# Performance work log

Hardware: AMD Instinct MI355X
Metric: run time of the kernel (lower is better)

## Reference

```python
import jax, jax.numpy as jnp
import numpy as np
from jax import lax

# ---- config (mirrors cfg) ----
NUM_LEVELS = 4
DS = 2            # DS_FACTOR
T = 16            # TILE_SIZE
SR = 4            # SEARCH_RADIUS
PADD = 1
SW = 0.1          # SPATIAL_WEIGHT
GR = 2            # GAUSS_RADIUS
SIGMA = 1.0
SS = 2 * (SR + PADD) + 1      # 11: padded search grid
SSC = 2 * SR + 1              # 9: cropped search grid
WIN = T + 2 * (SR + PADD)     # 26: gathered window per tile

# ---- subpixel-refinement quadratic-fit filters (from __init__) ----
F_A11 = jnp.asarray(np.array([[1,-2,1],[2,-4,2],[1,-2,1]], np.float32) / 4.0)
F_A22 = jnp.asarray(np.array([[1,2,1],[-2,-4,-2],[1,2,1]], np.float32) / 4.0)
F_A12 = jnp.asarray(np.array([[1,0,-1],[0,0,0],[-1,0,1]], np.float32) / 4.0)
F_B1  = jnp.asarray(np.array([[-1,0,1],[-2,0,2],[-1,0,1]], np.float32) / 8.0)
F_B2  = jnp.asarray(np.array([[-1,-2,-1],[0,0,0],[1,2,1]], np.float32) / 8.0)
F_C   = jnp.asarray(np.array([[-1,2,-1],[2,12,2],[-1,2,-1]], np.float32) / 16.0)


def _gauss_kernel():
    ws = 2 * GR + 1
    ax = np.arange(ws, dtype=np.float32) - GR
    g = np.exp(-(ax ** 2) / (2.0 * SIGMA ** 2))
    k = np.outer(g, g)
    k = k / k.sum()
    return jnp.asarray(k, jnp.float32)


def _pyramid(x):
    """Gaussian pyramid: depthwise gaussian blur + avg-pool(ds) per level."""
    k = _gauss_kernel()[None, None]  # OIHW, C=1
    pad = (2 * GR + 1 - 1) // 2
    pyr = [x]
    for _ in range(NUM_LEVELS - 1):
        y = lax.conv_general_dilated(x, k, (1, 1), [(pad, pad), (pad, pad)],
                                     dimension_numbers=('NCHW', 'OIHW', 'NCHW'))
        n, c, h, w = y.shape
        x = y.reshape(n, c, h // DS, DS, w // DS, DS).mean(axis=(3, 5))
        pyr.append(x)
    return pyr


def _sdist_map():
    ax = (np.arange(SS, dtype=np.float32) - (SR + PADD)) / float(SS)
    return jnp.asarray(ax[:, None] ** 2 + ax[None, :] ** 2, jnp.float32)


def _step(init_offset, src, dst):
    """One pyramid-level block-matching step + subpixel refine."""
    n, nth, ntw, _ = init_offset.shape
    H, W = src.shape[2], src.shape[3]
    oy = jnp.round(init_offset[..., 0]).astype(jnp.int32)
    ox = jnp.round(init_offset[..., 1]).astype(jnp.int32)
    base_y = (jnp.arange(nth, dtype=jnp.int32) * T)[None, :, None]
    base_x = (jnp.arange(ntw, dtype=jnp.int32) * T)[None, None, :]
    y0 = base_y + oy - (SR + PADD)
    x0 = base_x + ox - (SR + PADD)
    Y = jnp.clip(y0[..., None] + jnp.arange(WIN), 0, H - 1)
    X = jnp.clip(x0[..., None] + jnp.arange(WIN), 0, W - 1)
    nidx = jnp.arange(n)[:, None, None, None, None]
    window = dst[:, 0][nidx, Y[..., :, None], X[..., None, :]]
    # source tiles [n,nth,ntw,T,T]
    src_t = src[:, 0].reshape(n, nth, T, ntw, T).transpose(0, 1, 3, 2, 4)
    # all SSxSS candidate tiles from the window (static slide indices)
    sl = jnp.arange(SS)[:, None] + jnp.arange(T)[None, :]  # [SS,T]
    cand = window[:, :, :, sl[:, None, :, None], sl[None, :, None, :]]  # [n,nth,ntw,SS,SS,T,T]
    adist = jnp.mean((cand - src_t[:, :, :, None, None]) ** 2, axis=(-2, -1))
    dist_full = adist + SW * _sdist_map()  # [n,nth,ntw,SS,SS]
    dist = dist_full[:, :, :, PADD:-PADD, PADD:-PADD].reshape(n, nth, ntw, SSC * SSC)
    min_dist = jnp.min(dist, axis=3)
    pk = jnp.argmin(dist, axis=3)
    py = pk // SSC
    px = pk % SSC
    offset = init_offset + jnp.stack([(py - SR).astype(jnp.float32),
                                      (px - SR).astype(jnp.float32)], axis=3)
    # RegionSelection: 3x3 neighborhood of dist_full around (py+PADD, px+PADD)
    ry = (py + PADD)[..., None] + jnp.arange(-1, 2)
    rx = (px + PADD)[..., None] + jnp.arange(-1, 2)
    tyi = jnp.arange(nth)[None, :, None, None, None]
    txi = jnp.arange(ntw)[None, None, :, None, None]
    yreg = dist_full[nidx, tyi, txi, ry[..., :, None], rx[..., None, :]]  # [n,nth,ntw,3,3]
    s = lambda f: jnp.sum(f * yreg, axis=(-2, -1))
    a11 = jax.nn.relu(s(F_A11))
    a22 = jax.nn.relu(s(F_A22))
    a12 = s(F_A12)
    b1 = s(F_B1)
    b2 = s(F_B2)
    det = a11 * a22 - a12 ** 2
    a12z = jnp.where(det < 0, jnp.zeros_like(a12), a12)
    mu_x = -(a22 * b1 - a12z * b2) / det
    mu_y = -(a11 * b2 - a12z * b1) / det
    mu_len = jnp.sqrt(mu_y ** 2 + mu_x ** 2)
    dx = jnp.where(mu_len < 1.0, mu_x, jnp.zeros_like(mu_x))
    dy = jnp.where(mu_len < 1.0, mu_y, jnp.zeros_like(mu_y))
    offset = offset.at[..., 0].add(dy).at[..., 1].add(dx)
    return offset, min_dist


def _inherit(prev_offset, nth, ntw, H, W):
    typ = jnp.arange(nth) // DS
    txp = jnp.arange(ntw) // DS
    off = DS * prev_offset[:, typ[:, None], txp[None, :], :]
    iy = (jnp.arange(nth, dtype=jnp.float32) * T)[None, :, None]
    ix = (jnp.arange(ntw, dtype=jnp.float32) * T)[None, None, :]
    dy = jnp.clip(off[..., 0] + iy, 0.0, float(H - T)) - iy
    dx = jnp.clip(off[..., 1] + ix, 0.0, float(W - T)) - ix
    return jnp.round(jnp.stack([dy, dx], axis=3))


def _align(src, dst):
    ps = _pyramid(src)
    pd = _pyramid(dst)
    offset = None
    min_dist = None
    for level in range(NUM_LEVELS - 1, -1, -1):
        s, d = ps[level], pd[level]
        n, _, h, w = s.shape
        nth = int(np.ceil(h / T))
        ntw = int(np.ceil(w / T))
        if level == NUM_LEVELS - 1:
            init = jnp.zeros((n, nth, ntw, 2), jnp.float32)
        else:
            init = _inherit(offset, nth, ntw, h, w)
        offset, min_dist = _step(init, s, d)
    # nearest-neighbor upsample by TILE_SIZE to per-pixel maps
    pixel_off = jnp.repeat(jnp.repeat(offset, T, axis=1), T, axis=2)   # [n,H,W,2]
    pixel_dist = jnp.repeat(jnp.repeat(min_dist, T, axis=1), T, axis=2)  # [n,H,W]
    return pixel_off, pixel_dist


def setup_inputs() -> dict:
    key = jax.random.key(0)
    k1, k2 = jax.random.split(key)
    src = jax.random.uniform(k1, (4, 1, 512, 512), jnp.float32)
    dst = jax.random.uniform(k2, (4, 1, 512, 512), jnp.float32)
    return {"src": src, "dst": dst}


def reference(src, dst):
    return _align(src, dst)
```

## Files before the change

### kernel.cpp

```cpp
#include <hip/hip_runtime.h>


#define NB 4
#define NPIX (NB * 512 * 512)

constexpr float H6[6] = {
    0.027244342f, 0.149345013f, 0.323410645f,
    0.323410645f, 0.149345013f, 0.027244342f
};

__global__ void __launch_bounds__(256, 4)
pyramid_kernel(const float* __restrict__ src, const float* __restrict__ dst,
               float* __restrict__ ws) {
    __shared__ float smem[5520];
    float* patch = smem;
    float* tmpH1 = smem + 3840;
    float* l1    = smem;
    float* tmpH2 = smem + 784;
    float* l2    = smem + 1120;
    float* tmpH3 = smem + 1264;

    float* sL1 = ws;
    float* dL1 = sL1 + 4 * 65536;
    float* sL2 = dL1 + 4 * 65536;
    float* dL2 = sL2 + 4 * 16384;
    float* sL3 = dL2 + 4 * 16384;
    float* dL3 = sL3 + 4 * 4096;

    const int bx = blockIdx.x, by = blockIdx.y, z = blockIdx.z;
    const int t = threadIdx.x;
    const float* in = (z < 4) ? (src + (size_t)z * 262144) : (dst + (size_t)(z - 4) * 262144);
    float* oL1 = ((z < 4) ? sL1 : dL1) + (size_t)(z & 3) * 65536;
    float* oL2 = ((z < 4) ? sL2 : dL2) + (size_t)(z & 3) * 16384;
    float* oL3 = ((z < 4) ? sL3 : dL3) + (size_t)(z & 3) * 4096;

    {
        const int oy = by * 32 - 14, ox = bx * 32 - 14;
        for (int idx = t; idx < 3600; idx += 256) {
            int r = idx / 60, c = idx - r * 60;
            int gy = oy + r, gx = ox + c;
            float v = 0.f;
            if ((unsigned)gy < 512u && (unsigned)gx < 512u) v = in[gy * 512 + gx];
            patch[r * 64 + c] = v;
        }
    }
    __syncthreads();
    for (int idx = t; idx < 1680; idx += 256) {
        int r = idx / 28, v = idx - r * 28;
        const float* p = &patch[r * 64 + 2 * v];
        float a = 0.f;
        #pragma unroll
        for (int bq = 0; bq < 6; ++bq) a = fmaf(H6[bq], p[bq], a);
        tmpH1[r * 28 + v] = a;
    }
    __syncthreads();
    {
        const int oy = by * 16 - 6, ox = bx * 16 - 6;
        for (int idx = t; idx < 784; idx += 256) {
            int u = idx / 28, v = idx - u * 28;
            float a = 0.f;
            int y1 = oy + u, x1 = ox + v;
            if ((unsigned)y1 < 256u && (unsigned)x1 < 256u) {
                #pragma unroll
                for (int bq = 0; bq < 6; ++bq) a = fmaf(H6[bq], tmpH1[(2 * u + bq) * 28 + v], a);
            }
            l1[u * 28 + v] = a;
        }
    }
    __syncthreads();
    {
        int u = t >> 4, v = t & 15;
        oL1[(by * 16 + u) * 256 + bx * 16 + v] = l1[(6 + u) * 28 + 6 + v];
    }
    for (int idx = t; idx < 336; idx += 256) {
        int r = idx / 12, v = idx - r * 12;
        const float* p = &l1[r * 28 + 2 * v];
        float a = 0.f;
        #pragma unroll
        for (int bq = 0; bq < 6; ++bq) a = fmaf(H6[bq], p[bq], a);
        tmpH2[r * 12 + v] = a;
    }
    __syncthreads();
    {
        const int oy = by * 8 - 2, ox = bx * 8 - 2;
        if (t < 144) {
            int u = t / 12, v = t - u * 12;
            float a = 0.f;
            int y2 = oy + u, x2 = ox + v;
            if ((unsigned)y2 < 128u && (unsigned)x2 < 128u) {
                #pragma unroll
                for (int bq = 0; bq < 6; ++bq) a = fmaf(H6[bq], tmpH2[(2 * u + bq) * 12 + v], a);
            }
            l2[u * 12 + v] = a;
        }
    }
    __syncthreads();
    if (t < 64) {
        int u = t >> 3, v = t & 7;
        oL2[(by * 8 + u) * 128 + bx * 8 + v] = l2[(2 + u) * 12 + 2 + v];
    } else if (t < 112) {
        int idx = t - 64;
        int r = idx >> 2, v = idx & 3;
        const float* p = &l2[r * 12 + 2 * v];
        float a = 0.f;
        #pragma unroll
        for (int bq = 0; bq < 6; ++bq) a = fmaf(H6[bq], p[bq], a);
        tmpH3[r * 4 + v] = a;
    }
    __syncthreads();
    if (t < 16) {
        int u = t >> 2, v = t & 3;
        float a = 0.f;
        #pragma unroll
        for (int bq = 0; bq < 6; ++bq) a = fmaf(H6[bq], tmpH3[(2 * u + bq) * 4 + v], a);
        oL3[(by * 4 + u) * 64 + bx * 4 + v] = a;
    }
}

template<bool FULL>
__device__ __forceinline__ void do_level(const float* __restrict__ simg,
                                         const float* __restrict__ dimg, int H,
                                         int ty, int tx, float pary, float parx, bool first,
                                         float* win, float* st, float* dist, int lt,
                                         float& roy, float& rox, float& rod) {
    constexpr int NL = FULL ? 256 : 128;

    float dyf = 0.f, dxf = 0.f;
    if (!first) {
        float iy = (float)(ty * 16), ix = (float)(tx * 16);
        dyf = rintf(fminf(fmaxf(2.f * pary + iy, 0.f), (float)(H - 16)) - iy);
        dxf = rintf(fminf(fmaxf(2.f * parx + ix, 0.f), (float)(H - 16)) - ix);
    }
    const int ioy = (int)dyf, iox = (int)dxf;
    const int y0 = ty * 16 + ioy - 5;
    const int x0 = tx * 16 + iox - 5;

    for (int idx = lt; idx < 676; idx += NL) {
        int r = idx / 26, c = idx - r * 26;
        int gy = min(max(y0 + r, 0), H - 1);
        int gx = min(max(x0 + c, 0), H - 1);
        win[r * 28 + c] = dimg[gy * H + gx];
    }
    if (lt < 64) {
        int r = lt >> 2, q = lt & 3;
        const float4* srow = (const float4*)(simg + (size_t)(ty * 16 + r) * H + tx * 16);
        ((float4*)&st[r * 16])[q] = srow[q];
    }
    __syncthreads();

    const int dy = FULL ? (lt >> 4) : (lt >> 3);
    if (dy < 11) {
        float acc[11];
        #pragma unroll
        for (int q = 0; q < 11; ++q) acc[q] = 0.f;
        constexpr int ROWS = FULL ? 1 : 2;
        #pragma unroll
        for (int rr = 0; rr < ROWS; ++rr) {
            const int i = FULL ? (lt & 15) : ((lt & 7) * 2 + rr);
            float w[28], s[16];
            const float4* wp = (const float4*)&win[(dy + i) * 28];
            #pragma unroll
            for (int q = 0; q < 7; ++q) ((float4*)w)[q] = wp[q];
            const float4* sp = (const float4*)&st[i * 16];
            #pragma unroll
            for (int q = 0; q < 4; ++q) ((float4*)s)[q] = sp[q];
            #pragma unroll
            for (int dx = 0; dx < 11; ++dx) {
                #pragma unroll
                for (int j = 0; j < 16; ++j) {
                    float d = w[dx + j] - s[j];
                    acc[dx] = fmaf(d, d, acc[dx]);
                }
            }
        }
        constexpr int MMAX = FULL ? 8 : 4;
        #pragma unroll
        for (int m = 1; m <= MMAX; m <<= 1) {
            #pragma unroll
            for (int dx = 0; dx < 11; ++dx) acc[dx] += __shfl_xor(acc[dx], m);
        }
        const bool leader = FULL ? ((lt & 15) == 0) : ((lt & 7) == 0);
        if (leader) {
            float ay = (float)(dy - 5) * (1.f / 11.f);
            #pragma unroll
            for (int dx = 0; dx < 11; ++dx) {
                float ax = (float)(dx - 5) * (1.f / 11.f);
                dist[dy * 11 + dx] = acc[dx] * (1.f / 256.f) + 0.1f * (ay * ay + ax * ax);
            }
        }
    }
    __syncthreads();

    const int l = lt & 63;
    float bv; int bk;
    {
        int k = l;
        int py = k / 9, px = k - (k / 9) * 9;
        bv = dist[(py + 1) * 11 + (px + 1)]; bk = k;
        k = l + 64;
        if (k < 81) {
            py = k / 9; px = k - (k / 9) * 9;
            float d = dist[(py + 1) * 11 + (px + 1)];
            if (d < bv) { bv = d; bk = k; }
        }
    }
    #pragma unroll
    for (int m = 1; m <= 32; m <<= 1) {
        float ov = __shfl_xor(bv, m);
        int   ok = __shfl_xor(bk, m);
        if (ov < bv || (ov == bv && ok < bk)) { bv = ov; bk = ok; }
    }
    {
        int py = bk / 9, px = bk - (bk / 9) * 9;
        float y00 = dist[(py + 0) * 11 + (px + 0)], y01 = dist[(py + 0) * 11 + (px + 1)], y02 = dist[(py + 0) * 11 + (px + 2)];
        float y10 = dist[(py + 1) * 11 + (px + 0)], y11 = dist[(py + 1) * 11 + (px + 1)], y12 = dist[(py + 1) * 11 + (px + 2)];
        float y20 = dist[(py + 2) * 11 + (px + 0)], y21 = dist[(py + 2) * 11 + (px + 1)], y22 = dist[(py + 2) * 11 + (px + 2)];

        float a11 = (y00 - 2.f * y01 + y02 + 2.f * y10 - 4.f * y11 + 2.f * y12 + y20 - 2.f * y21 + y22) * 0.25f;
        a11 = fmaxf(a11, 0.f);
        float a22 = (y00 + 2.f * y01 + y02 - 2.f * y10 - 4.f * y11 - 2.f * y12 + y20 + 2.f * y21 + y22) * 0.25f;
        a22 = fmaxf(a22, 0.f);
        float a12 = (y00 - y02 - y20 + y22) * 0.25f;
        float b1  = (-y00 + y02 - 2.f * y10 + 2.f * y12 - y20 + y22) * 0.125f;
        float b2  = (-y00 - 2.f * y01 - y02 + y20 + 2.f * y21 + y22) * 0.125f;

        float det  = a11 * a22 - a12 * a12;
        float a12z = (det < 0.f) ? 0.f : a12;
        float mu_x = -(a22 * b1 - a12z * b2) / det;
        float mu_y = -(a11 * b2 - a12z * b1) / det;
        float mu_len = sqrtf(mu_x * mu_x + mu_y * mu_y);
        float addx = (mu_len < 1.f) ? mu_x : 0.f;
        float addy = (mu_len < 1.f) ? mu_y : 0.f;

        roy = dyf + (float)(py - 4) + addy;
        rox = dxf + (float)(px - 4) + addx;
        rod = bv;
    }
}

__global__ void __launch_bounds__(256, 4)
step_chain_kernel(const float* __restrict__ src, const float* __restrict__ dst,
                  const float* __restrict__ ws, float* __restrict__ out) {
    __shared__ float winS[2][26 * 28];
    __shared__ float stS[2][256];
    __shared__ float distS[2][128];

    const float* sL1 = ws;
    const float* dL1 = sL1 + 4 * 65536;
    const float* sL2 = dL1 + 4 * 65536;
    const float* dL2 = sL2 + 4 * 16384;
    const float* sL3 = dL2 + 4 * 16384;
    const float* dL3 = sL3 + 4 * 4096;

    const int gid = blockIdx.x;
    const int b   = gid >> 8;
    const int ty1 = (gid >> 4) & 15;
    const int tx1 = gid & 15;
    const int t    = threadIdx.x;
    const int slot = t >> 7;
    const int s_t  = t & 127;

    const float* s0 = src + (size_t)b * 262144; const float* d0 = dst + (size_t)b * 262144;
    const float* s1 = sL1 + (size_t)b * 65536;  const float* d1 = dL1 + (size_t)b * 65536;
    const float* s2 = sL2 + (size_t)b * 16384;  const float* d2 = dL2 + (size_t)b * 16384;
    const float* s3 = sL3 + (size_t)b * 4096;   const float* d3 = dL3 + (size_t)b * 4096;

    float oy, ox, od;
    do_level<true>(s3, d3,  64, ty1 >> 2, tx1 >> 2, 0.f, 0.f, true,
                   winS[0], stS[0], distS[0], t, oy, ox, od);
    do_level<true>(s2, d2, 128, ty1 >> 1, tx1 >> 1, oy, ox, false,
                   winS[0], stS[0], distS[0], t, oy, ox, od);
    do_level<true>(s1, d1, 256, ty1,      tx1,      oy, ox, false,
                   winS[0], stS[0], distS[0], t, oy, ox, od);
    const float s1y = oy, s1x = ox;

    #pragma unroll
    for (int half = 0; half < 2; ++half) {
        const int ty0 = 2 * ty1 + half, tx0 = 2 * tx1 + slot;
        do_level<false>(s0, d0, 512, ty0, tx0, s1y, s1x, false,
                        winS[slot], stS[slot], distS[slot], s_t, oy, ox, od);
        int r = s_t >> 3, c = (s_t & 7) * 2;
        int pyy = ty0 * 16 + r, pxx = tx0 * 16 + c;
        size_t pi = ((size_t)(b * 512 + pyy)) * 512 + pxx;
        float2 o; o.x = oy; o.y = ox;
        ((float2*)out)[pi]     = o;
        ((float2*)out)[pi + 1] = o;
        float2 dd; dd.x = od; dd.y = od;
        *(float2*)(out + (size_t)NPIX * 2 + pi) = dd;
    }
}

extern "C" void kernel_launch(void* const* d_in, const int* in_sizes, int n_in,
                              void* d_out, int out_size, void* d_ws, size_t ws_size,
                              hipStream_t stream) {
    const float* src = (const float*)d_in[0];
    const float* dst = (const float*)d_in[1];
    float* out = (float*)d_out;
    float* ws  = (float*)d_ws;

    hipLaunchKernelGGL(pyramid_kernel, dim3(16, 16, 8), dim3(256), 0, stream, src, dst, ws);
    hipLaunchKernelGGL(step_chain_kernel, dim3(1024), dim3(256), 0, stream, src, dst, ws, out);
}
```

Baseline: 112.1 us.

## Split step chain into per-level-0-tile blocks and fuse separable pyramid blur

The step chain kernel now launches one 128-thread block per finest-level tile. Each block recomputes the coarse levels 3, 2 and 1 redundantly, instead of sharing them across a 256-thread block that used two slots. This gives four times more blocks and removes the two-slot structure, at the cost of repeating the coarse-level work roughly fourfold. The pyramid kernel replaces its separable horizontal-then-vertical passes with a direct 6x6 2D filter, which drops the intermediate shared buffers and barriers but does more FMAs per output. It also raises the occupancy hint to 8 blocks.

```diff
diff --git a/kernel.cpp b/kernel.cpp
--- a/kernel.cpp
+++ b/kernel.cpp
@@ -9,16 +9,12 @@
     0.323410645f, 0.149345013f, 0.027244342f
 };
 
-__global__ void __launch_bounds__(256, 4)
+__global__ void __launch_bounds__(256, 8)
 pyramid_kernel(const float* __restrict__ src, const float* __restrict__ dst,
                float* __restrict__ ws) {
-    __shared__ float smem[5520];
-    float* patch = smem;
-    float* tmpH1 = smem + 3840;
-    float* l1    = smem;
-    float* tmpH2 = smem + 784;
-    float* l2    = smem + 1120;
-    float* tmpH3 = smem + 1264;
+    __shared__ float patch[60 * 64];
+    __shared__ float l1[28 * 28];
+    __shared__ float l2[12 * 12];
 
     float* sL1 = ws;
     float* dL1 = sL1 + 4 * 65536;
@@ -45,15 +41,6 @@
         }
     }
     __syncthreads();
-    for (int idx = t; idx < 1680; idx += 256) {
-        int r = idx / 28, v = idx - r * 28;
-        const float* p = &patch[r * 64 + 2 * v];
-        float a = 0.f;
-        #pragma unroll
-        for (int bq = 0; bq < 6; ++bq) a = fmaf(H6[bq], p[bq], a);
-        tmpH1[r * 28 + v] = a;
-    }
-    __syncthreads();
     {
         const int oy = by * 16 - 6, ox = bx * 16 - 6;
         for (int idx = t; idx < 784; idx += 256) {
@@ -62,7 +49,11 @@
             int y1 = oy + u, x1 = ox + v;
             if ((unsigned)y1 < 256u && (unsigned)x1 < 256u) {
                 #pragma unroll
-                for (int bq = 0; bq < 6; ++bq) a = fmaf(H6[bq], tmpH1[(2 * u + bq) * 28 + v], a);
+                for (int i = 0; i < 6; ++i) {
+                    const float* p = &patch[(2 * u + i) * 64 + 2 * v];
+                    #pragma unroll
+                    for (int j = 0; j < 6; ++j) a = fmaf(H6[i] * H6[j], p[j], a);
+                }
             }
             l1[u * 28 + v] = a;
         }
@@ -72,59 +63,44 @@
         int u = t >> 4, v = t & 15;
         oL1[(by * 16 + u) * 256 + bx * 16 + v] = l1[(6 + u) * 28 + 6 + v];
     }
-    for (int idx = t; idx < 336; idx += 256) {
-        int r = idx / 12, v = idx - r * 12;
-        const float* p = &l1[r * 28 + 2 * v];
+    if (t < 144) {
+        const int oy = by * 8 - 2, ox = bx * 8 - 2;
+        int u = t / 12, v = t - u * 12;
         float a = 0.f;
-        #pragma unroll
-        for (int bq = 0; bq < 6; ++bq) a = fmaf(H6[bq], p[bq], a);
-        tmpH2[r * 12 + v] = a;
-    }
-    __syncthreads();
-    {
-        const int oy = by * 8 - 2, ox = bx * 8 - 2;
-        if (t < 144) {
-            int u = t / 12, v = t - u * 12;
-            float a = 0.f;
-            int y2 = oy + u, x2 = ox + v;
-            if ((unsigned)y2 < 128u && (unsigned)x2 < 128u) {
+        int y2 = oy + u, x2 = ox + v;
+        if ((unsigned)y2 < 128u && (unsigned)x2 < 128u) {
+            #pragma unroll
+            for (int i = 0; i < 6; ++i) {
+                const float* p = &l1[(2 * u + i) * 28 + 2 * v];
                 #pragma unroll
-                for (int bq = 0; bq < 6; ++bq) a = fmaf(H6[bq], tmpH2[(2 * u + bq) * 12 + v], a);
-            }
-            l2[u * 12 + v] = a;
-        }
+                for (int j = 0; j < 6; ++j) a = fmaf(H6[i] * H6[j], p[j], a);
+            }
+        }
+        l2[u * 12 + v] = a;
     }
     __syncthreads();
     if (t < 64) {
         int u = t >> 3, v = t & 7;
         oL2[(by * 8 + u) * 128 + bx * 8 + v] = l2[(2 + u) * 12 + 2 + v];
-    } else if (t < 112) {
-        int idx = t - 64;
-        int r = idx >> 2, v = idx & 3;
-        const float* p = &l2[r * 12 + 2 * v];
+    } else if (t < 80) {
+        int k = t - 64;
+        int u = k >> 2, v = k & 3;
         float a = 0.f;
         #pragma unroll
-        for (int bq = 0; bq < 6; ++bq) a = fmaf(H6[bq], p[bq], a);
-        tmpH3[r * 4 + v] = a;
-    }
-    __syncthreads();
-    if (t < 16) {
-        int u = t >> 2, v = t & 3;
-        float a = 0.f;
-        #pragma unroll
-        for (int bq = 0; bq < 6; ++bq) a = fmaf(H6[bq], tmpH3[(2 * u + bq) * 4 + v], a);
+        for (int i = 0; i < 6; ++i) {
+            const float* p = &l2[(2 * u + i) * 12 + 2 * v];
+            #pragma unroll
+            for (int j = 0; j < 6; ++j) a = fmaf(H6[i] * H6[j], p[j], a);
+        }
         oL3[(by * 4 + u) * 64 + bx * 4 + v] = a;
     }
 }
 
-template<bool FULL>
 __device__ __forceinline__ void do_level(const float* __restrict__ simg,
                                          const float* __restrict__ dimg, int H,
                                          int ty, int tx, float pary, float parx, bool first,
                                          float* win, float* st, float* dist, int lt,
                                          float& roy, float& rox, float& rod) {
-    constexpr int NL = FULL ? 256 : 128;
-
     float dyf = 0.f, dxf = 0.f;
     if (!first) {
         float iy = (float)(ty * 16), ix = (float)(tx * 16);
@@ -135,7 +111,7 @@
     const int y0 = ty * 16 + ioy - 5;
     const int x0 = tx * 16 + iox - 5;
 
-    for (int idx = lt; idx < 676; idx += NL) {
+    for (int idx = lt; idx < 676; idx += 128) {
         int r = idx / 26, c = idx - r * 26;
         int gy = min(max(y0 + r, 0), H - 1);
         int gx = min(max(x0 + c, 0), H - 1);
@@ -148,15 +124,14 @@
     }
     __syncthreads();
 
-    const int dy = FULL ? (lt >> 4) : (lt >> 3);
+    const int dy = lt >> 3;
     if (dy < 11) {
         float acc[11];
         #pragma unroll
         for (int q = 0; q < 11; ++q) acc[q] = 0.f;
-        constexpr int ROWS = FULL ? 1 : 2;
-        #pragma unroll
-        for (int rr = 0; rr < ROWS; ++rr) {
-            const int i = FULL ? (lt & 15) : ((lt & 7) * 2 + rr);
+        #pragma unroll
+        for (int rr = 0; rr < 2; ++rr) {
+            const int i = (lt & 7) * 2 + rr;
             float w[28], s[16];
             const float4* wp = (const float4*)&win[(dy + i) * 28];
             #pragma unroll
@@ -173,14 +148,12 @@
                 }
             }
         }
-        constexpr int MMAX = FULL ? 8 : 4;
-        #pragma unroll
-        for (int m = 1; m <= MMAX; m <<= 1) {
+        #pragma unroll
+        for (int m = 1; m <= 4; m <<= 1) {
             #pragma unroll
             for (int dx = 0; dx < 11; ++dx) acc[dx] += __shfl_xor(acc[dx], m);
         }
-        const bool leader = FULL ? ((lt & 15) == 0) : ((lt & 7) == 0);
-        if (leader) {
+        if ((lt & 7) == 0) {
             float ay = (float)(dy - 5) * (1.f / 11.f);
             #pragma unroll
             for (int dx = 0; dx < 11; ++dx) {
@@ -238,12 +211,12 @@
     }
 }
 
-__global__ void __launch_bounds__(256, 4)
+__global__ void __launch_bounds__(128, 4)
 step_chain_kernel(const float* __restrict__ src, const float* __restrict__ dst,
                   const float* __restrict__ ws, float* __restrict__ out) {
-    __shared__ float winS[2][26 * 28];
-    __shared__ float stS[2][256];
-    __shared__ float distS[2][128];
+    __shared__ float win[26 * 28];
+    __shared__ float st[256];
+    __shared__ float dist[128];
 
     const float* sL1 = ws;
     const float* dL1 = sL1 + 4 * 65536;
@@ -253,12 +226,10 @@
     const float* dL3 = sL3 + 4 * 4096;
 
     const int gid = blockIdx.x;
-    const int b   = gid >> 8;
-    const int ty1 = (gid >> 4) & 15;
-    const int tx1 = gid & 15;
-    const int t    = threadIdx.x;
-    const int slot = t >> 7;
-    const int s_t  = t & 127;
+    const int b   = gid >> 10;
+    const int ty0 = (gid >> 5) & 31;
+    const int tx0 = gid & 31;
+    const int lt  = threadIdx.x;
 
     const float* s0 = src + (size_t)b * 262144; const float* d0 = dst + (size_t)b * 262144;
     const float* s1 = sL1 + (size_t)b * 65536;  const float* d1 = dL1 + (size_t)b * 65536;
@@ -266,28 +237,19 @@
     const float* s3 = sL3 + (size_t)b * 4096;   const float* d3 = dL3 + (size_t)b * 4096;
 
     float oy, ox, od;
-    do_level<true>(s3, d3,  64, ty1 >> 2, tx1 >> 2, 0.f, 0.f, true,
-                   winS[0], stS[0], distS[0], t, oy, ox, od);
-    do_level<true>(s2, d2, 128, ty1 >> 1, tx1 >> 1, oy, ox, false,
-                   winS[0], stS[0], distS[0], t, oy, ox, od);
-    do_level<true>(s1, d1, 256, ty1,      tx1,      oy, ox, false,
-                   winS[0], stS[0], distS[0], t, oy, ox, od);
-    const float s1y = oy, s1x = ox;
-
-    #pragma unroll
-    for (int half = 0; half < 2; ++half) {
-        const int ty0 = 2 * ty1 + half, tx0 = 2 * tx1 + slot;
-        do_level<false>(s0, d0, 512, ty0, tx0, s1y, s1x, false,
-                        winS[slot], stS[slot], distS[slot], s_t, oy, ox, od);
-        int r = s_t >> 3, c = (s_t & 7) * 2;
-        int pyy = ty0 * 16 + r, pxx = tx0 * 16 + c;
-        size_t pi = ((size_t)(b * 512 + pyy)) * 512 + pxx;
-        float2 o; o.x = oy; o.y = ox;
-        ((float2*)out)[pi]     = o;
-        ((float2*)out)[pi + 1] = o;
-        float2 dd; dd.x = od; dd.y = od;
-        *(float2*)(out + (size_t)NPIX * 2 + pi) = dd;
-    }
+    do_level(s3, d3,  64, ty0 >> 3, tx0 >> 3, 0.f, 0.f, true,  win, st, dist, lt, oy, ox, od);
+    do_level(s2, d2, 128, ty0 >> 2, tx0 >> 2, oy, ox, false, win, st, dist, lt, oy, ox, od);
+    do_level(s1, d1, 256, ty0 >> 1, tx0 >> 1, oy, ox, false, win, st, dist, lt, oy, ox, od);
+    do_level(s0, d0, 512, ty0,      tx0,      oy, ox, false, win, st, dist, lt, oy, ox, od);
+
+    int r = lt >> 3, c = (lt & 7) * 2;
+    int pyy = ty0 * 16 + r, pxx = tx0 * 16 + c;
+    size_t pi = ((size_t)(b * 512 + pyy)) * 512 + pxx;
+    float2 o; o.x = oy; o.y = ox;
+    ((float2*)out)[pi]     = o;
+    ((float2*)out)[pi + 1] = o;
+    float2 dd; dd.x = od; dd.y = od;
+    *(float2*)(out + (size_t)NPIX * 2 + pi) = dd;
 }
 
 extern "C" void kernel_launch(void* const* d_in, const int* in_sizes, int n_in,
@@ -299,5 +261,5 @@
     float* ws  = (float*)d_ws;
 
     hipLaunchKernelGGL(pyramid_kernel, dim3(16, 16, 8), dim3(256), 0, stream, src, dst, ws);
-    hipLaunchKernelGGL(step_chain_kernel, dim3(1024), dim3(256), 0, stream, src, dst, ws, out);
-}
+    hipLaunchKernelGGL(step_chain_kernel, dim3(4096), dim3(128), 0, stream, src, dst, ws, out);
+}
```

Result: slower. 140.8 us (+25.6%).

## Share one 42x44 window across four level-0 tiles when offsets are interior

Applied to the files above, without the earlier changes.

At level 0 the four child tiles inherit the same parent offset, so when the shifted 32x32 quad lies fully inside the image the block loads a single shared 42x44 destination window and a 32x32 source block. All 256 threads then compute the four tiles' cost maps together, followed by one wave-wide argmin and refine per tile, and outputs are written as float4. This is meant to cut redundant global gathers and barriers compared with two sequential half-block passes. Tiles near the border fall back to the old path, which adds code size and shared-memory aliasing complexity.

```diff
diff --git a/kernel.cpp b/kernel.cpp
--- a/kernel.cpp
+++ b/kernel.cpp
@@ -117,87 +117,46 @@
     }
 }
 
-template<bool FULL>
-__device__ __forceinline__ void do_level(const float* __restrict__ simg,
-                                         const float* __restrict__ dimg, int H,
-                                         int ty, int tx, float pary, float parx, bool first,
-                                         float* win, float* st, float* dist, int lt,
-                                         float& roy, float& rox, float& rod) {
-    constexpr int NL = FULL ? 256 : 128;
-
-    float dyf = 0.f, dxf = 0.f;
-    if (!first) {
-        float iy = (float)(ty * 16), ix = (float)(tx * 16);
-        dyf = rintf(fminf(fmaxf(2.f * pary + iy, 0.f), (float)(H - 16)) - iy);
-        dxf = rintf(fminf(fmaxf(2.f * parx + ix, 0.f), (float)(H - 16)) - ix);
-    }
-    const int ioy = (int)dyf, iox = (int)dxf;
-    const int y0 = ty * 16 + ioy - 5;
-    const int x0 = tx * 16 + iox - 5;
-
-    for (int idx = lt; idx < 676; idx += NL) {
-        int r = idx / 26, c = idx - r * 26;
-        int gy = min(max(y0 + r, 0), H - 1);
-        int gx = min(max(x0 + c, 0), H - 1);
-        win[r * 28 + c] = dimg[gy * H + gx];
-    }
-    if (lt < 64) {
-        int r = lt >> 2, q = lt & 3;
-        const float4* srow = (const float4*)(simg + (size_t)(ty * 16 + r) * H + tx * 16);
-        ((float4*)&st[r * 16])[q] = srow[q];
-    }
-    __syncthreads();
-
-    const int dy = FULL ? (lt >> 4) : (lt >> 3);
-    if (dy < 11) {
-        float acc[11];
-        #pragma unroll
-        for (int q = 0; q < 11; ++q) acc[q] = 0.f;
-        constexpr int ROWS = FULL ? 1 : 2;
-        #pragma unroll
-        for (int rr = 0; rr < ROWS; ++rr) {
-            const int i = FULL ? (lt & 15) : ((lt & 7) * 2 + rr);
-            float w[28], s[16];
-            const float4* wp = (const float4*)&win[(dy + i) * 28];
-            #pragma unroll
-            for (int q = 0; q < 7; ++q) ((float4*)w)[q] = wp[q];
-            const float4* sp = (const float4*)&st[i * 16];
-            #pragma unroll
-            for (int q = 0; q < 4; ++q) ((float4*)s)[q] = sp[q];
-            #pragma unroll
-            for (int dx = 0; dx < 11; ++dx) {
-                #pragma unroll
-                for (int j = 0; j < 16; ++j) {
-                    float d = w[dx + j] - s[j];
-                    acc[dx] = fmaf(d, d, acc[dx]);
-                }
-            }
-        }
-        constexpr int MMAX = FULL ? 8 : 4;
-        #pragma unroll
-        for (int m = 1; m <= MMAX; m <<= 1) {
-            #pragma unroll
-            for (int dx = 0; dx < 11; ++dx) acc[dx] += __shfl_xor(acc[dx], m);
-        }
-        const bool leader = FULL ? ((lt & 15) == 0) : ((lt & 7) == 0);
-        if (leader) {
-            float ay = (float)(dy - 5) * (1.f / 11.f);
-            #pragma unroll
-            for (int dx = 0; dx < 11; ++dx) {
-                float ax = (float)(dx - 5) * (1.f / 11.f);
-                dist[dy * 11 + dx] = acc[dx] * (1.f / 256.f) + 0.1f * (ay * ay + ax * ax);
-            }
-        }
-    }
-    __syncthreads();
-
-    const int l = lt & 63;
-    float bv; int bk;
+__device__ __forceinline__ void refine(const float* dist, int bk, float dyf, float dxf,
+                                       float& roy, float& rox) {
+    int py = bk / 9, px = bk - (bk / 9) * 9;
+    float y00 = dist[(py + 0) * 11 + (px + 0)], y01 = dist[(py + 0) * 11 + (px + 1)], y02 = dist[(py + 0) * 11 + (px + 2)];
+    float y10 = dist[(py + 1) * 11 + (px + 0)], y11 = dist[(py + 1) * 11 + (px + 1)], y12 = dist[(py + 1) * 11 + (px + 2)];
+    float y20 = dist[(py + 2) * 11 + (px + 0)], y21 = dist[(py + 2) * 11 + (px + 1)], y22 = dist[(py + 2) * 11 + (px + 2)];
+
+    float a11 = (y00 - 2.f * y01 + y02 + 2.f * y10 - 4.f * y11 + 2.f * y12 + y20 - 2.f * y21 + y22) * 0.25f;
+    a11 = fmaxf(a11, 0.f);
+    float a22 = (y00 + 2.f * y01 + y02 - 2.f * y10 - 4.f * y11 - 2.f * y12 + y20 + 2.f * y21 + y22) * 0.25f;
+    a22 = fmaxf(a22, 0.f);
+    float a12 = (y00 - y02 - y20 + y22) * 0.25f;
+    float b1  = (-y00 + y02 - 2.f * y10 + 2.f * y12 - y20 + y22) * 0.125f;
+    float b2  = (-y00 - 2.f * y01 - y02 + y20 + 2.f * y21 + y22) * 0.125f;
+
+    float det  = a11 * a22 - a12 * a12;
+    float a12z = (det < 0.f) ? 0.f : a12;
+    float mu_x = -(a22 * b1 - a12z * b2) / det;
+    float mu_y = -(a11 * b2 - a12z * b1) / det;
+    float mu_len = sqrtf(mu_x * mu_x + mu_y * mu_y);
+    float addx = (mu_len < 1.f) ? mu_x : 0.f;
+    float addy = (mu_len < 1.f) ? mu_y : 0.f;
+
+    roy = dyf + (float)(py - 4) + addy;
+    rox = dxf + (float)(px - 4) + addx;
+}
+
+__device__ __forceinline__ void inherit(int H, int ty, int tx, float pary, float parx,
+                                        float& dyf, float& dxf) {
+    float iy = (float)(ty * 16), ix = (float)(tx * 16);
+    dyf = rintf(fminf(fmaxf(2.f * pary + iy, 0.f), (float)(H - 16)) - iy);
+    dxf = rintf(fminf(fmaxf(2.f * parx + ix, 0.f), (float)(H - 16)) - ix);
+}
+
+__device__ __forceinline__ void argmin81(const float* dist, int lane, float& bv, int& bk) {
     {
-        int k = l;
+        int k = lane;
         int py = k / 9, px = k - (k / 9) * 9;
         bv = dist[(py + 1) * 11 + (px + 1)]; bk = k;
-        k = l + 64;
+        k = lane + 64;
         if (k < 81) {
             py = k / 9; px = k - (k / 9) * 9;
             float d = dist[(py + 1) * 11 + (px + 1)];
@@ -210,40 +169,157 @@
         int   ok = __shfl_xor(bk, m);
         if (ov < bv || (ov == bv && ok < bk)) { bv = ov; bk = ok; }
     }
-    {
-        int py = bk / 9, px = bk - (bk / 9) * 9;
-        float y00 = dist[(py + 0) * 11 + (px + 0)], y01 = dist[(py + 0) * 11 + (px + 1)], y02 = dist[(py + 0) * 11 + (px + 2)];
-        float y10 = dist[(py + 1) * 11 + (px + 0)], y11 = dist[(py + 1) * 11 + (px + 1)], y12 = dist[(py + 1) * 11 + (px + 2)];
-        float y20 = dist[(py + 2) * 11 + (px + 0)], y21 = dist[(py + 2) * 11 + (px + 1)], y22 = dist[(py + 2) * 11 + (px + 2)];
-
-        float a11 = (y00 - 2.f * y01 + y02 + 2.f * y10 - 4.f * y11 + 2.f * y12 + y20 - 2.f * y21 + y22) * 0.25f;
-        a11 = fmaxf(a11, 0.f);
-        float a22 = (y00 + 2.f * y01 + y02 - 2.f * y10 - 4.f * y11 - 2.f * y12 + y20 + 2.f * y21 + y22) * 0.25f;
-        a22 = fmaxf(a22, 0.f);
-        float a12 = (y00 - y02 - y20 + y22) * 0.25f;
-        float b1  = (-y00 + y02 - 2.f * y10 + 2.f * y12 - y20 + y22) * 0.125f;
-        float b2  = (-y00 - 2.f * y01 - y02 + y20 + 2.f * y21 + y22) * 0.125f;
-
-        float det  = a11 * a22 - a12 * a12;
-        float a12z = (det < 0.f) ? 0.f : a12;
-        float mu_x = -(a22 * b1 - a12z * b2) / det;
-        float mu_y = -(a11 * b2 - a12z * b1) / det;
-        float mu_len = sqrtf(mu_x * mu_x + mu_y * mu_y);
-        float addx = (mu_len < 1.f) ? mu_x : 0.f;
-        float addy = (mu_len < 1.f) ? mu_y : 0.f;
-
-        roy = dyf + (float)(py - 4) + addy;
-        rox = dxf + (float)(px - 4) + addx;
-        rod = bv;
-    }
+}
+
+__device__ __forceinline__ void full_level(const float* __restrict__ simg,
+                                           const float* __restrict__ dimg, int H,
+                                           int ty, int tx, float pary, float parx, bool first,
+                                           float* win, float* st, float* dist, int t,
+                                           float& roy, float& rox) {
+    float dyf = 0.f, dxf = 0.f;
+    if (!first) inherit(H, ty, tx, pary, parx, dyf, dxf);
+    const int ioy = (int)dyf, iox = (int)dxf;
+    const int y0 = ty * 16 + ioy - 5;
+    const int x0 = tx * 16 + iox - 5;
+
+    for (int idx = t; idx < 676; idx += 256) {
+        int r = idx / 26, c = idx - r * 26;
+        int gy = min(max(y0 + r, 0), H - 1);
+        int gx = min(max(x0 + c, 0), H - 1);
+        win[r * 28 + c] = dimg[gy * H + gx];
+    }
+    if (t < 64) {
+        int r = t >> 2, q = t & 3;
+        const float4* srow = (const float4*)(simg + (size_t)(ty * 16 + r) * H + tx * 16);
+        ((float4*)&st[r * 16])[q] = srow[q];
+    }
+    __syncthreads();
+
+    const int dy = t >> 4;
+    if (dy < 11) {
+        float acc[11];
+        #pragma unroll
+        for (int q = 0; q < 11; ++q) acc[q] = 0.f;
+        const int i = t & 15;
+        float w[28], s[16];
+        const float4* wp = (const float4*)&win[(dy + i) * 28];
+        #pragma unroll
+        for (int q = 0; q < 7; ++q) ((float4*)w)[q] = wp[q];
+        const float4* sp = (const float4*)&st[i * 16];
+        #pragma unroll
+        for (int q = 0; q < 4; ++q) ((float4*)s)[q] = sp[q];
+        #pragma unroll
+        for (int dx = 0; dx < 11; ++dx) {
+            #pragma unroll
+            for (int j = 0; j < 16; ++j) {
+                float d = w[dx + j] - s[j];
+                acc[dx] = fmaf(d, d, acc[dx]);
+            }
+        }
+        #pragma unroll
+        for (int m = 1; m <= 8; m <<= 1) {
+            #pragma unroll
+            for (int dx = 0; dx < 11; ++dx) acc[dx] += __shfl_xor(acc[dx], m);
+        }
+        if ((t & 15) == 0) {
+            float ay = (float)(dy - 5) * (1.f / 11.f);
+            #pragma unroll
+            for (int dx = 0; dx < 11; ++dx) {
+                float ax = (float)(dx - 5) * (1.f / 11.f);
+                dist[dy * 11 + dx] = acc[dx] * (1.f / 256.f) + 0.1f * (ay * ay + ax * ax);
+            }
+        }
+    }
+    __syncthreads();
+
+    float bv; int bk;
+    argmin81(dist, t & 63, bv, bk);
+    refine(dist, bk, dyf, dxf, roy, rox);
+}
+
+__device__ __forceinline__ void half_level(const float* __restrict__ simg,
+                                           const float* __restrict__ dimg, int H,
+                                           int ty, int tx, float pary, float parx,
+                                           float* win, float* st, float* dist, int lt,
+                                           float& roy, float& rox, float& rod) {
+    float dyf, dxf;
+    inherit(H, ty, tx, pary, parx, dyf, dxf);
+    const int ioy = (int)dyf, iox = (int)dxf;
+    const int y0 = ty * 16 + ioy - 5;
+    const int x0 = tx * 16 + iox - 5;
+
+    for (int idx = lt; idx < 676; idx += 128) {
+        int r = idx / 26, c = idx - r * 26;
+        int gy = min(max(y0 + r, 0), H - 1);
+        int gx = min(max(x0 + c, 0), H - 1);
+        win[r * 28 + c] = dimg[gy * H + gx];
+    }
+    if (lt < 64) {
+        int r = lt >> 2, q = lt & 3;
+        const float4* srow = (const float4*)(simg + (size_t)(ty * 16 + r) * H + tx * 16);
+        ((float4*)&st[r * 16])[q] = srow[q];
+    }
+    __syncthreads();
+
+    const int dy = lt >> 3;
+    if (dy < 11) {
+        float acc[11];
+        #pragma unroll
+        for (int q = 0; q < 11; ++q) acc[q] = 0.f;
+        #pragma unroll
+        for (int rr = 0; rr < 2; ++rr) {
+            const int i = (lt & 7) * 2 + rr;
+            float w[28], s[16];
+            const float4* wp = (const float4*)&win[(dy + i) * 28];
+            #pragma unroll
+            for (int q = 0; q < 7; ++q) ((float4*)w)[q] = wp[q];
+            const float4* sp = (const float4*)&st[i * 16];
+            #pragma unroll
+            for (int q = 0; q < 4; ++q) ((float4*)s)[q] = sp[q];
+            #pragma unroll
+            for (int dx = 0; dx < 11; ++dx) {
+                #pragma unroll
+                for (int j = 0; j < 16; ++j) {
+                    float d = w[dx + j] - s[j];
+                    acc[dx] = fmaf(d, d, acc[dx]);
+                }
+            }
+        }
+        #pragma unroll
+        for (int m = 1; m <= 4; m <<= 1) {
+            #pragma unroll
+            for (int dx = 0; dx < 11; ++dx) acc[dx] += __shfl_xor(acc[dx], m);
+        }
+        if ((lt & 7) == 0) {
+            float ay = (float)(dy - 5) * (1.f / 11.f);
+            #pragma unroll
+            for (int dx = 0; dx < 11; ++dx) {
+                float ax = (float)(dx - 5) * (1.f / 11.f);
+                dist[dy * 11 + dx] = acc[dx] * (1.f / 256.f) + 0.1f * (ay * ay + ax * ax);
+            }
+        }
+    }
+    __syncthreads();
+
+    float bv; int bk;
+    argmin81(dist, lt & 63, bv, bk);
+    refine(dist, bk, dyf, dxf, roy, rox);
+    rod = bv;
 }
 
 __global__ void __launch_bounds__(256, 4)
 step_chain_kernel(const float* __restrict__ src, const float* __restrict__ dst,
                   const float* __restrict__ ws, float* __restrict__ out) {
-    __shared__ float winS[2][26 * 28];
-    __shared__ float stS[2][256];
-    __shared__ float distS[2][128];
+    __shared__ float pool[3384];
+    float* winF  = pool;
+    float* stF   = pool + 784;
+    float* winS1 = pool + 1040;
+    float* stS1  = pool + 1824;
+    float* win42 = pool;
+    float* stQ   = pool + 1848;
+    float* distQ = pool + 2872;
+    float* dist0 = pool + 2872;
+    float* dist1 = pool + 3000;
 
     const float* sL1 = ws;
     const float* dL1 = sL1 + 4 * 65536;
@@ -256,37 +332,118 @@
     const int b   = gid >> 8;
     const int ty1 = (gid >> 4) & 15;
     const int tx1 = gid & 15;
-    const int t    = threadIdx.x;
-    const int slot = t >> 7;
-    const int s_t  = t & 127;
+    const int t   = threadIdx.x;
 
     const float* s0 = src + (size_t)b * 262144; const float* d0 = dst + (size_t)b * 262144;
     const float* s1 = sL1 + (size_t)b * 65536;  const float* d1 = dL1 + (size_t)b * 65536;
     const float* s2 = sL2 + (size_t)b * 16384;  const float* d2 = dL2 + (size_t)b * 16384;
     const float* s3 = sL3 + (size_t)b * 4096;   const float* d3 = dL3 + (size_t)b * 4096;
 
-    float oy, ox, od;
-    do_level<true>(s3, d3,  64, ty1 >> 2, tx1 >> 2, 0.f, 0.f, true,
-                   winS[0], stS[0], distS[0], t, oy, ox, od);
-    do_level<true>(s2, d2, 128, ty1 >> 1, tx1 >> 1, oy, ox, false,
-                   winS[0], stS[0], distS[0], t, oy, ox, od);
-    do_level<true>(s1, d1, 256, ty1,      tx1,      oy, ox, false,
-                   winS[0], stS[0], distS[0], t, oy, ox, od);
-    const float s1y = oy, s1x = ox;
-
-    #pragma unroll
-    for (int half = 0; half < 2; ++half) {
-        const int ty0 = 2 * ty1 + half, tx0 = 2 * tx1 + slot;
-        do_level<false>(s0, d0, 512, ty0, tx0, s1y, s1x, false,
-                        winS[slot], stS[slot], distS[slot], s_t, oy, ox, od);
-        int r = s_t >> 3, c = (s_t & 7) * 2;
-        int pyy = ty0 * 16 + r, pxx = tx0 * 16 + c;
-        size_t pi = ((size_t)(b * 512 + pyy)) * 512 + pxx;
-        float2 o; o.x = oy; o.y = ox;
-        ((float2*)out)[pi]     = o;
-        ((float2*)out)[pi + 1] = o;
-        float2 dd; dd.x = od; dd.y = od;
-        *(float2*)(out + (size_t)NPIX * 2 + pi) = dd;
+    float oy, ox;
+    full_level(s3, d3,  64, ty1 >> 2, tx1 >> 2, 0.f, 0.f, true,  winF, stF, dist0, t, oy, ox);
+    full_level(s2, d2, 128, ty1 >> 1, tx1 >> 1, oy, ox, false, winF, stF, dist0, t, oy, ox);
+    full_level(s1, d1, 256, ty1,      tx1,      oy, ox, false, winF, stF, dist0, t, oy, ox);
+
+    const float cy = 2.f * oy + (float)(ty1 * 32);
+    const float cx = 2.f * ox + (float)(tx1 * 32);
+    const bool fastq = (cy >= 0.f) && (cy + 16.f <= 496.f) &&
+                       (cx >= 0.f) && (cx + 16.f <= 496.f);
+
+    if (fastq) {
+        const float dyf = rintf(2.f * oy), dxf = rintf(2.f * ox);
+        const int Y0 = ty1 * 32 + (int)dyf - 5;
+        const int X0 = tx1 * 32 + (int)dxf - 5;
+
+        for (int idx = t; idx < 1848; idx += 256) {
+            int r = idx / 44, c = idx - r * 44;
+            int gy = min(max(Y0 + r, 0), 511);
+            int gx = min(max(X0 + c, 0), 511);
+            win42[idx] = d0[gy * 512 + gx];
+        }
+        {
+            int r = t >> 3, q = t & 7;
+            const float4* srow = (const float4*)(s0 + (size_t)(ty1 * 32 + r) * 512 + tx1 * 32);
+            ((float4*)&stQ[r * 32])[q] = srow[q];
+        }
+        __syncthreads();
+
+        const int dy = t >> 4;
+        const int i  = t & 15;
+        if (dy < 11) {
+            #pragma unroll
+            for (int c = 0; c < 4; ++c) {
+                const int rb = (c >> 1) * 16, cb = (c & 1) * 16;
+                float acc[11];
+                #pragma unroll
+                for (int q = 0; q < 11; ++q) acc[q] = 0.f;
+                float w[28], s[16];
+                const float4* wp = (const float4*)&win42[(rb + dy + i) * 44 + cb];
+                #pragma unroll
+                for (int q = 0; q < 7; ++q) ((float4*)w)[q] = wp[q];
+                const float4* sp = (const float4*)&stQ[(rb + i) * 32 + cb];
+                #pragma unroll
+                for (int q = 0; q < 4; ++q) ((float4*)s)[q] = sp[q];
+                #pragma unroll
+                for (int dx = 0; dx < 11; ++dx) {
+                    #pragma unroll
+                    for (int j = 0; j < 16; ++j) {
+                        float d = w[dx + j] - s[j];
+                        acc[dx] = fmaf(d, d, acc[dx]);
+                    }
+                }
+                #pragma unroll
+                for (int m = 1; m <= 8; m <<= 1) {
+                    #pragma unroll
+                    for (int dx = 0; dx < 11; ++dx) acc[dx] += __shfl_xor(acc[dx], m);
+                }
+                if (i == 0) {
+                    float ay = (float)(dy - 5) * (1.f / 11.f);
+                    #pragma unroll
+                    for (int dx = 0; dx < 11; ++dx) {
+                        float ax = (float)(dx - 5) * (1.f / 11.f);
+                        distQ[c * 128 + dy * 11 + dx] = acc[dx] * (1.f / 256.f) + 0.1f * (ay * ay + ax * ax);
+                    }
+                }
+            }
+        }
+        __syncthreads();
+
+        const int w    = t >> 6;
+        const int lane = t & 63;
+        const float* dc = &distQ[w * 128];
+        float bv; int bk;
+        argmin81(dc, lane, bv, bk);
+        float coy, cox;
+        refine(dc, bk, dyf, dxf, coy, cox);
+
+        const int ty0 = 2 * ty1 + (w >> 1), tx0 = 2 * tx1 + (w & 1);
+        int r = lane >> 2, c = (lane & 3) * 4;
+        size_t pi = ((size_t)(b * 512 + ty0 * 16 + r)) * 512 + tx0 * 16 + c;
+        float4 o2; o2.x = coy; o2.y = cox; o2.z = coy; o2.w = cox;
+        float4* po = (float4*)(out + 2 * pi);
+        po[0] = o2; po[1] = o2;
+        float4 dd; dd.x = bv; dd.y = bv; dd.z = bv; dd.w = bv;
+        *(float4*)(out + (size_t)NPIX * 2 + pi) = dd;
+    } else {
+        const int slot = t >> 7;
+        const int s_t  = t & 127;
+        float* win  = slot ? winS1 : winF;
+        float* st   = slot ? stS1  : stF;
+        float* dist = slot ? dist1 : dist0;
+
+        #pragma unroll
+        for (int half = 0; half < 2; ++half) {
+            const int ty0 = 2 * ty1 + half, tx0 = 2 * tx1 + slot;
+            float coy, cox, od;
+            half_level(s0, d0, 512, ty0, tx0, oy, ox, win, st, dist, s_t, coy, cox, od);
+            int r = s_t >> 3, c = (s_t & 7) * 2;
+            size_t pi = ((size_t)(b * 512 + ty0 * 16 + r)) * 512 + tx0 * 16 + c;
+            float2 o; o.x = coy; o.y = cox;
+            ((float2*)out)[pi]     = o;
+            ((float2*)out)[pi + 1] = o;
+            float2 dd; dd.x = od; dd.y = od;
+            *(float2*)(out + (size_t)NPIX * 2 + pi) = dd;
+        }
     }
 }
 
```

Result: no change. 112.4 us (+0.2%).
